# Optimization experiments

Measured on AMD Instinct MI355X. Metric: run time of the kernel, lower is better.

The kernel has to match this reference:

```python
import jax, jax.numpy as jnp
import numpy as np

T = 1 << 20  # hash-table size for bilateral-grid vertices
PRIMES = jnp.array([73856093, 19349663, 83492791, 49979687, 24036583], dtype=jnp.int32)
RGB2YUV = jnp.array([[0.299, 0.587, 0.114], [-0.168736, -0.331264, 0.5], [0.5, -0.418688, -0.081312]], dtype=jnp.float32)
YUV_OFF = jnp.array([0.0, 128.0, 128.0], dtype=jnp.float32)
SIG = jnp.array([8.0, 2.0, 2.0], dtype=jnp.float32)  # sigma_luma, sigma_chroma, sigma_chroma (mode=0)
SIGMA_SPATIAL = 7.0
LAM = 200.0
A_DIAG_MIN = 1e-5
CG_MAXITER = 12
BISTO_ITERS = 10
EPS = 1e-12
DIM = 5


def _hash(c):  # (..., 5) int32 -> flat bin id in [0, T)
    return (c * PRIMES).sum(-1) & (T - 1)


def _norm_max(x):
    s = jnp.clip(jnp.max(x, axis=(1, 2, 3), keepdims=True), 1e-5, 1.0)
    return x / s


def _conv(x, w, b, stride, pad):
    y = jax.lax.conv_general_dilated(x, w, (stride, stride), ((pad, pad), (pad, pad)), dimension_numbers=('NCHW', 'OIHW', 'NCHW'))
    return y + b[None, :, None, None]


def _gn(x, g, b, groups=2, eps=1e-5):
    B, C, H, W = x.shape
    xg = x.reshape(B, groups, -1)
    mu = xg.mean(-1, keepdims=True)
    var = xg.var(-1, keepdims=True)
    xg = (xg - mu) * jax.lax.rsqrt(var + eps)
    return xg.reshape(B, C, H, W) * g[None, :, None, None] + b[None, :, None, None]


def _reppad(x):
    return jnp.pad(x, ((0, 0), (0, 0), (1, 1), (1, 1)), mode='edge')


def _resize(x, h, w):
    B, C = x.shape[:2]
    return jax.image.resize(x, (B, C, h, w), method='linear')


def _bilateral_solve(guide_hwc, target_hwc, conf_hw):
    # fast bilateral solver (Barron & Poole): splat -> bistochastize -> PCG on grid -> slice
    H, W, C = target_hwc.shape
    N = H * W
    yuv = guide_hwc.reshape(N, 3) @ RGB2YUV.T + YUV_OFF
    yy, xx = jnp.meshgrid(jnp.arange(H, dtype=jnp.float32), jnp.arange(W, dtype=jnp.float32), indexing='ij')
    sp = jnp.stack([xx, yy], -1).reshape(N, 2) / SIGMA_SPATIAL
    coords = jnp.concatenate([jnp.floor(sp), jnp.floor(yuv / SIG)], -1).astype(jnp.int32)  # (N,5)
    h = _hash(coords)
    occ = jnp.zeros((T,), bool).at[h].set(True)
    ctab = jnp.full((T, 5), -1, jnp.int32).at[h].set(coords)
    # precompute 1-2-1 blur neighbor gathers along each of the 5 grid dims
    nhs, vals = [], []
    for d in range(DIM):
        for off in (-1, 1):
            nc = ctab.at[:, d].add(off)
            nh = _hash(nc)
            nhs.append(nh)
            vals.append(occ & occ[nh] & jnp.all(ctab[nh] == nc, axis=-1))
    occf = occ[:, None]

    def blur(v):  # (T,k)
        out = (2.0 * DIM) * v
        for nh, va in zip(nhs, vals):
            out = out + jnp.where(va[:, None], v[nh], 0.0)
        return jnp.where(occf, out, 0.0)

    def splat(v):  # (N,k) -> (T,k)
        return jax.ops.segment_sum(v, h, num_segments=T)

    # bistochastization
    m = splat(jnp.ones((N, 1), jnp.float32))
    n = occf.astype(jnp.float32)
    for _ in range(BISTO_ITERS):
        n = jnp.sqrt(n * m / (blur(n) + EPS))
    m = n * blur(n)

    w = conf_hw.reshape(N, 1)
    w_splat = splat(w)
    b = splat(w * target_hwc.reshape(N, C))
    y0 = b / (w_splat + EPS)
    A_diag = jnp.maximum(LAM * (m - (2.0 * DIM) * n * n) + w_splat, A_DIAG_MIN)
    Minv = 1.0 / A_diag

    def A(v):  # A = lam*(Dm - Dn B Dn) + diag(splat(w))
        return LAM * (m * v - n * blur(n * v)) + w_splat * v

    x0 = y0
    r0 = b - A(x0)
    z0 = Minv * r0

    def step(st, _):
        x, r, z, p = st
        Ap = A(p)
        rz = (r * z).sum(0)
        alpha = rz / ((p * Ap).sum(0) + EPS)
        x = x + alpha * p
        r = r - alpha * Ap
        z = Minv * r
        beta = (r * z).sum(0) / (rz + EPS)
        p = z + beta * p
        return (x, r, z, p), None

    (x, _, _, _), _ = jax.lax.scan(step, (x0, r0, z0, z0), None, length=CG_MAXITER)
    return x[h].reshape(H, W, C)  # slice


def _forward(image, feature, pred, w1, b1, g1, be1, w2, b2, g2, be2, wd1, bd1, gd1, bed1, wd2, bd2, gd2, bed2, wf, bf):
    image = _norm_max(image)
    feature = _norm_max(feature)
    inp = jax.lax.stop_gradient(jnp.concatenate([image, pred], axis=1))
    x1 = jax.nn.relu(_gn(_conv(_reppad(inp), w1, b1, 2, 0), g1, be1))
    x2 = jax.nn.relu(_gn(_conv(_reppad(x1), w2, b2, 2, 0), g2, be2))
    dx1 = jax.nn.relu(_gn(_conv(x2, wd1, bd1, 1, 1), gd1, bed1))
    dx1 = _resize(dx1, x1.shape[2], x1.shape[3])
    dx2 = jax.nn.relu(_gn(_conv(jnp.concatenate([dx1, x1], 1), wd2, bd2, 1, 1), gd2, bed2))
    dx2 = _resize(dx2, inp.shape[2], inp.shape[3])
    conf = 0.5 * (jnp.tanh(_conv(_reppad(dx2), wf, bf, 1, 0)) + 1.0)
    conf = conf / jnp.maximum(conf.max(), 1e-5)
    guide = jax.lax.stop_gradient(feature) * 255.0
    out = jax.vmap(_bilateral_solve)(guide.transpose(0, 2, 3, 1), pred.transpose(0, 2, 3, 1), conf[:, 0])
    return out.transpose(0, 3, 1, 2), conf


def setup_inputs():
    key = jax.random.key(0)
    ks = jax.random.split(key, 8)
    B, H, W = 2, 384, 512

    def cw(k, shape, fan_in):
        return jax.random.normal(k, shape, jnp.float32) * (1.0 / np.sqrt(fan_in))

    return {
        'image': jax.random.uniform(ks[0], (B, 3, H, W), jnp.float32),
        'feature': jax.random.uniform(ks[1], (B, 3, H, W), jnp.float32),
        'pred': jax.random.uniform(ks[2], (B, 3, H, W), jnp.float32),
        'w1': cw(ks[3], (16, 6, 4, 4), 6 * 16), 'b1': jnp.zeros((16,), jnp.float32),
        'g1': jnp.ones((16,), jnp.float32), 'be1': jnp.zeros((16,), jnp.float32),
        'w2': cw(ks[4], (16, 16, 4, 4), 16 * 16), 'b2': jnp.zeros((16,), jnp.float32),
        'g2': jnp.ones((16,), jnp.float32), 'be2': jnp.zeros((16,), jnp.float32),
        'wd1': cw(ks[5], (16, 16, 3, 3), 16 * 9), 'bd1': jnp.zeros((16,), jnp.float32),
        'gd1': jnp.ones((16,), jnp.float32), 'bed1': jnp.zeros((16,), jnp.float32),
        'wd2': cw(ks[6], (16, 32, 3, 3), 32 * 9), 'bd2': jnp.zeros((16,), jnp.float32),
        'gd2': jnp.ones((16,), jnp.float32), 'bed2': jnp.zeros((16,), jnp.float32),
        'wf': cw(ks[7], (1, 16, 3, 3), 16 * 9), 'bf': jnp.zeros((1,), jnp.float32),
    }


def reference(image, feature, pred, w1, b1, g1, be1, w2, b2, g2, be2, wd1, bd1, gd1, bed1, wd2, bd2, gd2, bed2, wf, bf):
    return _forward(image, feature, pred, w1, b1, g1, be1, w2, b2, g2, be2, wd1, bd1, gd1, bed1, wd2, bd2, gd2, bed2, wf, bf)
```

## Files before the change

### kernel.cpp

```cpp
#include <hip/hip_runtime.h>

#define H_ 384
#define W_ 512
#define N_ (H_*W_)
#define B_ 2
#define T_ 1048576
#define TMASK_ 0xFFFFFu
#define G2N_ ((2*N_)/256)
#define G2T_ ((2*T_)/256)
#define CHS_ 64
#define RZ0_ 192
#define RZB_ 2688
#define PAP0_ 5568
#define PAPB_ 2496
#define GN0_ 10560

__device__ __forceinline__ int prime(int d){
  switch(d){
    case 0: return 73856093;
    case 1: return 19349663;
    case 2: return 83492791;
    case 3: return 49979687;
    default: return 24036583;
  }
}

__device__ __forceinline__ float clampScale(float s){ return fminf(fmaxf(s,1e-5f),1.0f); }

__device__ __forceinline__ double blockReduceD(double v){
  __shared__ double sh[4];
  for(int s=32;s>0;s>>=1) v += __shfl_down(v,s,64);
  int lane=threadIdx.x&63, w=threadIdx.x>>6;
  if(lane==0) sh[w]=v;
  __syncthreads();
  double r = sh[0]+sh[1]+sh[2]+sh[3];
  __syncthreads();
  return r;
}
__device__ __forceinline__ float blockReduceMaxF(float v){
  __shared__ float sh[4];
  for(int s=32;s>0;s>>=1) v = fmaxf(v,__shfl_down(v,s,64));
  int lane=threadIdx.x&63, w=threadIdx.x>>6;
  if(lane==0) sh[w]=v;
  __syncthreads();
  float r = fmaxf(fmaxf(sh[0],sh[1]),fmaxf(sh[2],sh[3]));
  __syncthreads();
  return r;
}

__device__ __forceinline__ void redAdd(double* base, int c, double v){
  atomicAdd(&base[c*CHS_ + ((blockIdx.x&7)<<3)], v);
}
__device__ __forceinline__ float redSum(const double* base, int c){
  double s=0.0;
  #pragma unroll
  for(int j=0;j<8;j++) s += base[c*CHS_ + j*8];
  return (float)s;
}

__device__ __forceinline__ void gnStats(const double* acc, int b, int c, double len,
                                        float* mf, float* rs){
  const double* ba = acc + (b*2 + (c>>3))*128;
  double s=0.0,s2=0.0;
  #pragma unroll
  for(int j=0;j<8;j++){ s+=ba[j*8]; s2+=ba[64+j*8]; }
  double mean = s/len;
  double var = s2/len - mean*mean;
  *rs = (float)(1.0/sqrt(var + 1e-5));
  *mf = (float)mean;
}


__global__ __launch_bounds__(256) void k_maxes(const float4* img4, const float4* feat4, float* scal){
  const int PB = (3*N_)/4;
  for(int b=0;b<2;b++){
    float lm=0.f, lf=0.f;
    for(int idx = blockIdx.x*256+threadIdx.x; idx<PB; idx += gridDim.x*256){
      float4 a=img4[(size_t)b*PB+idx], c=feat4[(size_t)b*PB+idx];
      lm=fmaxf(lm, fmaxf(fmaxf(a.x,a.y),fmaxf(a.z,a.w)));
      lf=fmaxf(lf, fmaxf(fmaxf(c.x,c.y),fmaxf(c.z,c.w)));
    }
    lm=blockReduceMaxF(lm); lf=blockReduceMaxF(lf);
    if(threadIdx.x==0){
      atomicMax((int*)&scal[b],   __float_as_int(lm));
      atomicMax((int*)&scal[2+b], __float_as_int(lf));
    }
  }
}

template<int PLANE4>
__global__ __launch_bounds__(256) void k_gnrelu(const float4* in, float4* out, const double* acc,
                                                const float* gamma, const float* beta){
  int idx = blockIdx.x*256 + threadIdx.x;
  int t = idx / PLANE4;
  int c = t & 15, b = t >> 4;
  __shared__ float smf, srs, sg, sbe;
  if(threadIdx.x==0){
    float mf, rs;
    gnStats(acc, b, c, 8.0*(double)(PLANE4*4), &mf, &rs);
    smf=mf; srs=rs; sg=gamma[c]; sbe=beta[c];
  }
  __syncthreads();
  float mf=smf, rs=srs, g=sg, be=sbe;
  float4 v = in[idx];
  v.x = fmaxf((v.x-mf)*rs*g+be, 0.f);
  v.y = fmaxf((v.y-mf)*rs*g+be, 0.f);
  v.z = fmaxf((v.z-mf)*rs*g+be, 0.f);
  v.w = fmaxf((v.w-mf)*rs*g+be, 0.f);
  out[idx] = v;
}

template<bool SCALEA,int NCH,int K,int S,bool EDGE,int IH,int IW,int NOC>
__device__ __forceinline__ void conv_accum(const float* __restrict__ plane0, int icBase, float mulA,
                                           int oy, int ox, const float* wlds, float acc[NOC]){
  for(int ic=0; ic<NCH; ic++){
    const float* plane = plane0 + (size_t)ic*IH*IW;
    #pragma unroll
    for(int ky=0;ky<K;ky++){
      int iy = oy*S + ky - 1;
      int cy = min(max(iy,0),IH-1);
      bool yin = (iy>=0)&&(iy<IH);
      const float* row = plane + cy*IW;
      #pragma unroll
      for(int kx=0;kx<K;kx++){
        int ix = ox*S + kx - 1;
        float v;
        if(EDGE){
          int cx = min(max(ix,0),IW-1);
          v = row[cx];
          if(SCALEA) v = v * mulA;
        } else {
          bool inb = yin && ix>=0 && ix<IW;
          if(inb){
            v = row[ix];
            if(SCALEA) v = v * mulA;
          } else v = 0.f;
        }
        const float* wp = &wlds[((icBase+ic)*K*K + ky*K + kx)*NOC];
        #pragma unroll
        for(int q=0;q<NOC;q++) acc[q] += v*wp[q];
      }
    }
  }
}

template<bool SCALEA,int ICA,int ICB,int K,int S,bool EDGE,int IH,int IW,int OH,int OW,int OCSPLIT>
__global__ __launch_bounds__(256) void k_convT(const float* __restrict__ inA, const float* __restrict__ inB,
                        const float* __restrict__ wt, const float* __restrict__ bias,
                        float* __restrict__ out, double* gnaccOut, const float* scal){
  constexpr int IC = ICA+ICB;
  constexpr int NOC = 16/OCSPLIT;
  constexpr int PB = (B_*OH*OW)/256;
  __shared__ float wlds[IC*K*K*NOC];
  __shared__ float blds[NOC];
  int pb  = blockIdx.x % PB;
  int ocg = blockIdx.x / PB;
  int ocBase = ocg*NOC;
  for(int i=threadIdx.x; i<IC*K*K*NOC; i+=256){
    int q = i % NOC, ickk = i / NOC;
    wlds[i] = wt[(ocBase+q)*IC*K*K + ickk];
  }
  if(threadIdx.x<NOC) blds[threadIdx.x]=bias[ocBase+threadIdx.x];
  __syncthreads();
  int idx = pb*256+threadIdx.x;
  int ox = idx % OW; int t=idx/OW; int oy=t%OH; int b=t/OH;
  float mulA = SCALEA ? 1.0f/clampScale(scal[b]) : 1.0f;
  float acc[NOC];
  #pragma unroll
  for(int q=0;q<NOC;q++) acc[q]=0.f;
  conv_accum<SCALEA,ICA,K,S,EDGE,IH,IW,NOC>(inA + (size_t)b*ICA*IH*IW, 0, mulA, oy, ox, wlds, acc);
  if constexpr(ICB>0)
    conv_accum<false,(ICB>0?ICB:1),K,S,EDGE,IH,IW,NOC>(inB + (size_t)b*ICB*IH*IW, ICA, 1.0f, oy, ox, wlds, acc);
  double s=0.0,s2=0.0;
  #pragma unroll
  for(int q=0;q<NOC;q++){
    float vv = acc[q] + blds[q];
    out[(((size_t)b*16+(ocBase+q))*OH+oy)*OW+ox] = vv;
    s += vv; s2 += (double)vv*(double)vv;
  }
  s=blockReduceD(s); s2=blockReduceD(s2);
  if(threadIdx.x==0){
    int grp = ocBase>>3;
    int sub = (blockIdx.x&7)<<3;
    atomicAdd(&gnaccOut[(b*2+grp)*128 + sub],      s);
    atomicAdd(&gnaccOut[(b*2+grp)*128 + 64 + sub], s2);
  }
}

template<int IH,int IW>
__global__ __launch_bounds__(256) void k_resize2x(const float* __restrict__ in, float* __restrict__ out,
                                                  const double* acc, const float* gamma, const float* beta){
  constexpr int QP = IH*IW;
  constexpr int OW = 2*IW;
  int idx = blockIdx.x*256 + threadIdx.x;
  int q = idx % QP; int t = idx / QP;
  int qx = q % IW, qy = q / IW;
  int c = t & 15, b = t >> 4;
  __shared__ float smf, srs, sg, sbe;
  if(threadIdx.x==0){
    float mf, rs;
    gnStats(acc, b, c, 8.0*(double)QP, &mf, &rs);
    smf=mf; srs=rs; sg=gamma[c]; sbe=beta[c];
  }
  __syncthreads();
  float mf=smf, rs=srs, g=sg, be=sbe;
  const float* plane = in + (size_t)t*QP;
  int ym = max(qy-1,0), yp = min(qy+1,IH-1);
  int xm = max(qx-1,0), xp = min(qx+1,IW-1);
  const float* r0 = plane + ym*IW;
  const float* r1 = plane + qy*IW;
  const float* r2 = plane + yp*IW;
  float a00=fmaxf((r0[xm]-mf)*rs*g+be,0.f), a01=fmaxf((r0[qx]-mf)*rs*g+be,0.f), a02=fmaxf((r0[xp]-mf)*rs*g+be,0.f);
  float a10=fmaxf((r1[xm]-mf)*rs*g+be,0.f), a11=fmaxf((r1[qx]-mf)*rs*g+be,0.f), a12=fmaxf((r1[xp]-mf)*rs*g+be,0.f);
  float a20=fmaxf((r2[xm]-mf)*rs*g+be,0.f), a21=fmaxf((r2[qx]-mf)*rs*g+be,0.f), a22=fmaxf((r2[xp]-mf)*rs*g+be,0.f);
  float e0 = 0.25f*a00+0.75f*a01, o0 = 0.75f*a01+0.25f*a02;
  float e1 = 0.25f*a10+0.75f*a11, o1 = 0.75f*a11+0.25f*a12;
  float e2 = 0.25f*a20+0.75f*a21, o2 = 0.75f*a21+0.25f*a22;
  float2 rE = make_float2(0.25f*e0+0.75f*e1, 0.25f*o0+0.75f*o1);
  float2 rO = make_float2(0.75f*e1+0.25f*e2, 0.75f*o1+0.25f*o2);
  float* po = out + (size_t)t*(4*QP) + (size_t)(2*qy)*OW + 2*qx;
  *(float2*)po        = rE;
  *(float2*)(po + OW) = rO;
}

__global__ __launch_bounds__(256) void k_conv5(const float* in, const float* wf, const float* bf,
                                               float* confr, float* scal){
  int idx = blockIdx.x*256 + threadIdx.x;
  int ph = idx % (N_/2); int b = idx / (N_/2);
  int oyh = ph / W_, ox = ph % W_;
  int oy0 = oyh*2;
  float acc0 = bf[0], acc1 = bf[0];
  for(int ic=0; ic<16; ic++){
    const float* plane = in + ((size_t)b*16+ic)*N_;
    #pragma unroll
    for(int ky=0;ky<3;ky++){
      int iy0 = min(max(oy0+ky-1,0),H_-1);
      int iy1 = min(max(oy0+ky,0),H_-1);
      const float* row0 = plane + iy0*W_;
      const float* row1 = plane + iy1*W_;
      #pragma unroll
      for(int kx=0;kx<3;kx++){
        int ix = min(max(ox+kx-1,0),W_-1);
        float w = wf[(ic*3+ky)*3+kx];
        acc0 += row0[ix]*w;
        acc1 += row1[ix]*w;
      }
    }
  }
  float c0 = 0.5f*(tanhf(acc0)+1.0f);
  float c1 = 0.5f*(tanhf(acc1)+1.0f);
  confr[(size_t)b*N_ + oy0*W_ + ox]     = c0;
  confr[(size_t)b*N_ + (oy0+1)*W_ + ox] = c1;
  float mx = blockReduceMaxF(fmaxf(c0,c1));
  if(threadIdx.x==0) atomicMax((int*)&scal[4], __float_as_int(mx));
}


__global__ __launch_bounds__(256) void k_px1(const float* feat, const float* scal,
                                             int* hpix, int2* cpix2, int* winner,
                                             float* mcompE, float4* splatE4){
  int idx = blockIdx.x*256 + threadIdx.x;
  int b = idx / N_, pix = idx % N_;
  int y = pix / W_, x = pix % W_;
  mcompE[idx] = 0.f;
  splatE4[idx] = make_float4(0.f,0.f,0.f,0.f);
  float sF = clampScale(scal[2+b]);
  const float* fb = feat + (size_t)b*3*N_;
  float R  = __fmul_rn(__fdiv_rn(fb[pix],      sF), 255.0f);
  float G  = __fmul_rn(__fdiv_rn(fb[N_+pix],   sF), 255.0f);
  float Bl = __fmul_rn(__fdiv_rn(fb[2*N_+pix], sF), 255.0f);
  float Y = __fadd_rn(__fadd_rn(__fadd_rn(__fmul_rn(0.299f,R),     __fmul_rn(0.587f,G)),  __fmul_rn(0.114f,Bl)), 0.0f);
  float U = __fadd_rn(__fadd_rn(__fadd_rn(__fmul_rn(-0.168736f,R), __fmul_rn(-0.331264f,G)), __fmul_rn(0.5f,Bl)), 128.0f);
  float V = __fadd_rn(__fadd_rn(__fadd_rn(__fmul_rn(0.5f,R),       __fmul_rn(-0.418688f,G)), __fmul_rn(-0.081312f,Bl)), 128.0f);
  int c[5];
  c[0] = (int)floorf(__fdiv_rn((float)x, 7.0f));
  c[1] = (int)floorf(__fdiv_rn((float)y, 7.0f));
  c[2] = (int)floorf(__fdiv_rn(Y, 8.0f));
  c[3] = (int)floorf(__fdiv_rn(U, 2.0f));
  c[4] = (int)floorf(__fdiv_rn(V, 2.0f));
  unsigned hh = 0;
  #pragma unroll
  for(int d=0;d<5;d++) hh += (unsigned)c[d]*(unsigned)prime(d);
  hh &= TMASK_;
  hpix[idx]=(int)hh;
  cpix2[idx]=make_int2(c[0] | (c[1]<<10) | (c[2]<<20), c[3] | (c[4]<<10));
  atomicMax(&winner[(size_t)b*T_+(int)hh], pix);
}


__global__ __launch_bounds__(256) void k_cnt(const int* winner, int* bcnt){
  int t = blockIdx.x*256 + threadIdx.x;
  bool occ = winner[t] >= 0;
  __shared__ int wc[4];
  unsigned long long mk = __ballot(occ);
  int lane = threadIdx.x & 63, w = threadIdx.x >> 6;
  if(lane==0) wc[w] = __popcll(mk);
  __syncthreads();
  if(threadIdx.x==0) bcnt[blockIdx.x] = wc[0]+wc[1]+wc[2]+wc[3];
}

__global__ __launch_bounds__(256) void k_scan(const int* bcnt, int* boff, int* count){
  __shared__ int ssum[256];
  int t = threadIdx.x;
  int base = t*32;
  int loc[32];
  int s=0;
  #pragma unroll
  for(int j=0;j<32;j++){ loc[j]=s; s+=bcnt[base+j]; }
  int mys = s;
  ssum[t]=s;
  __syncthreads();
  for(int st=1; st<128; st<<=1){
    int add = ((t&127) >= st) ? ssum[t-st] : 0;
    __syncthreads();
    ssum[t] += add;
    __syncthreads();
  }
  int excl = ssum[t] - mys;
  #pragma unroll
  for(int j=0;j<32;j++) boff[base+j] = excl + loc[j];
  if(t==127) count[0]=ssum[127];
  if(t==255) count[1]=ssum[255];
}

__global__ __launch_bounds__(256) void k_cmp(const int* winner, const int* boff,
                                             int2* cidx2, int* slot_of){
  int t = blockIdx.x*256 + threadIdx.x;
  int b = t / T_;
  int wn = winner[t];
  bool occ = wn >= 0;
  __shared__ int wc[4];
  unsigned long long mk = __ballot(occ);
  int lane = threadIdx.x & 63, w = threadIdx.x >> 6;
  if(lane==0) wc[w] = __popcll(mk);
  __syncthreads();
  int wpre = 0;
  for(int k2=0;k2<4;k2++) if(k2<w) wpre += wc[k2];
  if(occ){
    int li = boff[blockIdx.x] + wpre + __popcll(mk & ((1ull<<lane)-1ull));
    int gi = b*N_ + li;
    cidx2[t] = make_int2(gi, wn);
    slot_of[gi] = t - b*T_;
  } else {
    cidx2[t] = make_int2(-1, -1);
  }
}

__global__ __launch_bounds__(256) void k_px3(int* hpix_gpix, const int2* cidx2, const float* confr,
                                             const float* scal, float* confout, const float* pred,
                                             float* mcomp, float4* splat4, float* mcompE, float* splatE){
  int idx = blockIdx.x*256 + threadIdx.x;
  int b = idx / N_, pix = idx % N_;
  int2 cw = cidx2[(size_t)b*T_ + hpix_gpix[idx]];
  int gi = cw.x;
  hpix_gpix[idx] = gi;
  float w = confr[idx] / fmaxf(scal[4], 1e-5f);
  confout[idx] = w;
  const float* pb = pred + (size_t)b*3*N_;
  float v0 = __fmul_rn(w, pb[pix]);
  float v1 = __fmul_rn(w, pb[N_+pix]);
  float v2 = __fmul_rn(w, pb[2*N_+pix]);
  if(cw.y == pix){
    splat4[gi] = make_float4(v0,v1,v2,w);
    mcomp[gi] = 1.0f;
  } else {
    float* s = splatE + 4*(size_t)gi;
    atomicAdd(s+0, v0);
    atomicAdd(s+1, v1);
    atomicAdd(s+2, v2);
    atomicAdd(s+3, w);
    atomicAdd(&mcompE[gi], 1.0f);
  }
}


__global__ __launch_bounds__(256) void k_bisto0(const int* count, const int* slot_of,
                      const int2* cpix2, const int2* cidx2, int* nbr,
                      float* mcomp, const float* mcompE, float4* splat4, const float4* splatE4,
                      float* nd){
  int i = blockIdx.x*256 + threadIdx.x;
  int b = i / N_, li = i - b*N_;
  if(li >= count[b]) return;
  int hh = slot_of[i];
  const int2* c2b = cidx2 + (size_t)b*T_;
  int2 cself = c2b[hh];
  int2 cp = cpix2[(size_t)b*N_ + cself.y];
  float4 sp = splat4[i]; float4 se = splatE4[i];
  sp.x+=se.x; sp.y+=se.y; sp.z+=se.z; sp.w+=se.w;
  splat4[i]=sp;
  float mTot = mcomp[i] + mcompE[i];
  mcomp[i]=mTot;
  float bv = 10.f;
  #pragma unroll
  for(int j=0;j<10;j++){
    int d=j>>1; int off=(j&1)?1:-1;
    unsigned nh = ((unsigned)hh + (unsigned)(off*prime(d))) & TMASK_;
    int nb = -1;
    int2 cn2 = c2b[nh];
    if(cn2.y>=0){
      int2 cn = cpix2[(size_t)b*N_ + cn2.y];
      int e0 = cp.x + (d==0?off: d==1?off*(1<<10) : d==2?off*(1<<20) : 0);
      int e1 = cp.y + (d==3?off: d==4?off*(1<<10) : 0);
      if(cn.x==e0 && cn.y==e1) nb = cn2.x;
    }
    nbr[(size_t)j*(2*N_)+i]=nb;
    if(nb>=0) bv += 1.0f;
  }
  nd[i] = sqrtf(1.0f*mTot/(bv+1e-12f));
}

__global__ __launch_bounds__(256) void k_bisto(const int* count, const int* nbr,
                                               const float* ns, float* nd, const float* mc){
  int i = blockIdx.x*256 + threadIdx.x;
  int b = i / N_, li = i - b*N_;
  if(li >= count[b]) return;
  float nv = ns[i];
  float bv = 10.f*nv;
  #pragma unroll
  for(int j=0;j<10;j++){
    int nb = nbr[(size_t)j*(2*N_)+i];
    if(nb>=0) bv += ns[nb];
  }
  nd[i] = sqrtf(nv*mc[i]/(bv+1e-12f));
}

__global__ __launch_bounds__(256) void k_Ar0(const int* count, const int* nbr, const float* n,
                      const float4* splat4, float4* meta4, float4* x4, float4* rS, float4* zp0,
                      double* rz0){
  int i = blockIdx.x*256 + threadIdx.x;
  int b = i / N_, li = i - b*N_;
  double a0=0.0,a1=0.0,a2=0.0;
  if(li < count[b]){
    float4 vb4 = splat4[i];
    float wsi = vb4.w;
    float nv = n[i];
    float x0 = vb4.x/(wsi+1e-12f);
    float x1 = vb4.y/(wsi+1e-12f);
    float x2 = vb4.z/(wsi+1e-12f);
    float bv = 10.f*nv;
    float s0=10.f*(nv*x0), s1=10.f*(nv*x1), s2=10.f*(nv*x2);
    #pragma unroll
    for(int j=0;j<10;j++){
      int nb = nbr[(size_t)j*(2*N_)+i];
      if(nb>=0){
        float4 vbn = splat4[nb];
        float nn = n[nb];
        bv += nn;
        s0 += nn*(vbn.x/(vbn.w+1e-12f));
        s1 += nn*(vbn.y/(vbn.w+1e-12f));
        s2 += nn*(vbn.z/(vbn.w+1e-12f));
      }
    }
    float mfin = nv*bv;
    float Ad = fmaxf(200.0f*(mfin - 10.f*nv*nv) + wsi, 1e-5f);
    float mi = 1.0f/Ad;
    float A0 = 200.f*(mfin*x0 - nv*s0) + wsi*x0;
    float A1 = 200.f*(mfin*x1 - nv*s1) + wsi*x1;
    float A2 = 200.f*(mfin*x2 - nv*s2) + wsi*x2;
    float r0v = vb4.x-A0, r1v = vb4.y-A1, r2v = vb4.z-A2;
    float z0=mi*r0v, z1=mi*r1v, z2=mi*r2v;
    meta4[i]=make_float4(nv,mfin,wsi,mi);
    x4[i]=make_float4(x0,x1,x2,0.f);
    rS[i]=make_float4(r0v,r1v,r2v,mi);
    zp0[2*(size_t)i]   = make_float4(z0,z1,z2,mi);
    zp0[2*(size_t)i+1] = make_float4(z0,z1,z2,nv);
    a0=(double)r0v*z0; a1=(double)r1v*z1; a2=(double)r2v*z2;
  }
  a0=blockReduceD(a0); a1=blockReduceD(a1); a2=blockReduceD(a2);
  if(threadIdx.x==0){
    double* base = rz0 + b*RZB_;
    redAdd(base,0,a0); redAdd(base,1,a1); redAdd(base,2,a2);
  }
}

__global__ __launch_bounds__(256) void k_Ap(const int* count, const int* nbr, const float4* meta4,
                     const float4* __restrict__ zpCur, float4* __restrict__ zpNext, float4* Ap4,
                     const double* bNum, const double* bDen, int bstr, double* pAp){
  int i = blockIdx.x*256 + threadIdx.x;
  int b = (blockIdx.x*256) / N_;
  int li = i - b*N_;
  __shared__ float sbe[3];
  if(threadIdx.x==0){
    if(bstr==0){ sbe[0]=0.f; sbe[1]=0.f; sbe[2]=0.f; }
    else{
      const double* nB_ = bNum + b*bstr;
      const double* dB_ = bDen + b*bstr;
      #pragma unroll
      for(int c=0;c<3;c++) sbe[c] = redSum(nB_,c) / (redSum(dB_,c)+1e-12f);
    }
  }
  __syncthreads();
  float be0=sbe[0], be1=sbe[1], be2=sbe[2];
  double a0=0.0,a1=0.0,a2=0.0;
  if(li < count[b]){
    float4 mt = meta4[i];
    float nv = mt.x, mfin = mt.y, wsi = mt.z;
    float4 zs = zpCur[2*(size_t)i];
    float4 ps = zpCur[2*(size_t)i+1];
    float p0 = zs.x + be0*ps.x;
    float p1 = zs.y + be1*ps.y;
    float p2 = zs.z + be2*ps.z;
    float s0=10.f*(nv*p0), s1=10.f*(nv*p1), s2=10.f*(nv*p2);
    #pragma unroll
    for(int j=0;j<10;j++){
      int nb = nbr[(size_t)j*(2*N_)+i];
      if(nb>=0){
        float4 zn = zpCur[2*(size_t)nb];
        float4 pn = zpCur[2*(size_t)nb+1];
        float nn = pn.w;
        s0 += nn*(zn.x + be0*pn.x);
        s1 += nn*(zn.y + be1*pn.y);
        s2 += nn*(zn.z + be2*pn.z);
      }
    }
    float A0 = 200.f*(mfin*p0 - nv*s0) + wsi*p0;
    float A1 = 200.f*(mfin*p1 - nv*s1) + wsi*p1;
    float A2 = 200.f*(mfin*p2 - nv*s2) + wsi*p2;
    zpNext[2*(size_t)i+1]=make_float4(p0,p1,p2,nv);
    Ap4[i]=make_float4(A0,A1,A2,0.f);
    a0=(double)p0*A0; a1=(double)p1*A1; a2=(double)p2*A2;
  }
  a0=blockReduceD(a0); a1=blockReduceD(a1); a2=blockReduceD(a2);
  if(threadIdx.x==0){
    double* base = pAp + b*PAPB_;
    redAdd(base,0,a0); redAdd(base,1,a1); redAdd(base,2,a2);
  }
}

__global__ __launch_bounds__(256) void k_upd1(const int* count, float4* x4, float4* rS,
                       const float4* __restrict__ zpNext_p, float4* __restrict__ zpNext_z,
                       const float4* Ap4,
                       const double* rzCur, const double* pApC, double* rzNew, int doRz){
  int i = blockIdx.x*256 + threadIdx.x;
  int b = (blockIdx.x*256) / N_;
  int li = i - b*N_;
  __shared__ float sal[3];
  if(threadIdx.x==0){
    const double* rc = rzCur + b*RZB_;
    const double* pc = pApC  + b*PAPB_;
    #pragma unroll
    for(int c=0;c<3;c++) sal[c] = redSum(rc,c) / (redSum(pc,c)+1e-12f);
  }
  __syncthreads();
  float al0=sal[0], al1=sal[1], al2=sal[2];
  double a0=0.0,a1=0.0,a2=0.0;
  if(li < count[b]){
    float4 xv = x4[i];
    float4 rv = rS[i];
    float4 pv = zpNext_p[2*(size_t)i+1];
    float4 av = Ap4[i];
    float mi = rv.w;
    float x0=xv.x+al0*pv.x, x1=xv.y+al1*pv.y, x2=xv.z+al2*pv.z;
    float r0v=rv.x-al0*av.x, r1v=rv.y-al1*av.y, r2v=rv.z-al2*av.z;
    float z0=mi*r0v, z1=mi*r1v, z2=mi*r2v;
    x4[i]=make_float4(x0,x1,x2,0.f);
    rS[i]=make_float4(r0v,r1v,r2v,mi);
    zpNext_z[2*(size_t)i]=make_float4(z0,z1,z2,mi);
    a0=(double)r0v*z0; a1=(double)r1v*z1; a2=(double)r2v*z2;
  }
  if(doRz){
    a0=blockReduceD(a0); a1=blockReduceD(a1); a2=blockReduceD(a2);
    if(threadIdx.x==0){
      double* base = rzNew + b*RZB_;
      redAdd(base,0,a0); redAdd(base,1,a1); redAdd(base,2,a2);
    }
  }
}

__global__ __launch_bounds__(256) void k_out(const float4* x4, const int* gpix, float* out){
  int idx = blockIdx.x*256 + threadIdx.x;
  int b = idx / N_, pix = idx % N_;
  float4 xv = x4[gpix[idx]];
  out[((size_t)(b*3+0))*N_+pix] = xv.x;
  out[((size_t)(b*3+1))*N_+pix] = xv.y;
  out[((size_t)(b*3+2))*N_+pix] = xv.z;
}


extern "C" void kernel_launch(void* const* d_in, const int* in_sizes, int n_in,
                              void* d_out, int out_size, void* d_ws, size_t ws_size,
                              hipStream_t stream){
  const float* image=(const float*)d_in[0];
  const float* feature=(const float*)d_in[1];
  const float* pred=(const float*)d_in[2];
  const float* w1=(const float*)d_in[3];  const float* b1=(const float*)d_in[4];
  const float* g1=(const float*)d_in[5];  const float* be1=(const float*)d_in[6];
  const float* w2=(const float*)d_in[7];  const float* b2=(const float*)d_in[8];
  const float* g2=(const float*)d_in[9];  const float* be2=(const float*)d_in[10];
  const float* wd1=(const float*)d_in[11];const float* bd1=(const float*)d_in[12];
  const float* gd1=(const float*)d_in[13];const float* bed1=(const float*)d_in[14];
  const float* wd2=(const float*)d_in[15];const float* bd2=(const float*)d_in[16];
  const float* gd2=(const float*)d_in[17];const float* bed2=(const float*)d_in[18];
  const float* wf=(const float*)d_in[19]; const float* bf=(const float*)d_in[20];
  float* outp=(float*)d_out;
  float* confout = outp + (size_t)B_*3*N_;

  char* wsb=(char*)d_ws;
  float* scal=(float*)wsb;
  int* count=(int*)(wsb+256);
  double* scalD=(double*)(wsb+4096);
  double* zeroD = scalD;
  auto rzArr  = [&](int it)->double*{ return scalD + RZ0_  + it*192; };
  auto pApArr = [&](int it)->double*{ return scalD + PAP0_ + it*192; };
  auto gnAcc  = [&](int L)->double*{ return scalD + GN0_ + L*512; };

  size_t off = 131072;
  auto alloc=[&](size_t bytes)->char*{ char* pp=wsb+off; off=(off+bytes+255)&~(size_t)255; return pp; };
  const size_t ALLOC0 = off;

  float* x1   =(float*)alloc((size_t)B_*16*192*256*4);
  float* x1n  =(float*)alloc((size_t)B_*16*192*256*4);
  float* x2   =(float*)alloc((size_t)B_*16*96*128*4);
  float* x2n  =(float*)alloc((size_t)B_*16*96*128*4);
  float* dx1  =(float*)alloc((size_t)B_*16*96*128*4);
  float* dx1r =(float*)alloc((size_t)B_*16*192*256*4);
  float* dx2  =(float*)alloc((size_t)B_*16*192*256*4);
  float* dx2r =(float*)alloc((size_t)B_*16*N_*4);

  off = ALLOC0;
  int*    winner =(int*)   alloc((size_t)2*T_*4);
  int2*   cidx2  =(int2*)  alloc((size_t)2*T_*8);
  int*    hpix   =(int*)   alloc((size_t)2*N_*4);
  int2*   cpix2  =(int2*)  alloc((size_t)2*N_*8);
  int*    slot_of=(int*)   alloc((size_t)2*N_*4);
  int*    nbr    =(int*)   alloc((size_t)2*N_*10*4);
  float*  mcomp  =(float*) alloc((size_t)2*N_*4);
  float4* splat4 =(float4*)alloc((size_t)2*N_*16);
  float*  mcompE =(float*) alloc((size_t)2*N_*4);
  float*  splatE =(float*) alloc((size_t)2*N_*16);
  float*  nA     =(float*) alloc((size_t)2*N_*4);
  float*  nB     =(float*) alloc((size_t)2*N_*4);
  float4* meta4  =(float4*)alloc((size_t)2*N_*16);
  float4* x4     =(float4*)alloc((size_t)2*N_*16);
  float4* rS     =(float4*)alloc((size_t)2*N_*16);
  float4* zpA4   =(float4*)alloc((size_t)2*N_*32);
  float4* zpB4   =(float4*)alloc((size_t)2*N_*32);
  int*    bcnt   =(int*)   alloc((size_t)G2T_*4);
  int*    boff   =(int*)   alloc((size_t)G2T_*4);
  float4* Ap4    = splat4;
  float*  confr  = (float*)zpB4;

  dim3 blk(256);

  hipMemsetAsync(wsb, 0, 4096 + 12608*8, stream);

  k_maxes<<<128,blk,0,stream>>>((const float4*)image,(const float4*)feature,scal);

  k_convT<true,3,3,4,2,true,384,512,192,256,4><<<4*((B_*192*256)/256),blk,0,stream>>>(
      image,pred,w1,b1,x1,gnAcc(0),scal);
  k_gnrelu<12288><<<(B_*16*12288)/256,blk,0,stream>>>((const float4*)x1,(float4*)x1n,gnAcc(0),g1,be1);
  k_convT<false,16,0,4,2,true,192,256,96,128,8><<<8*((B_*96*128)/256),blk,0,stream>>>(
      x1n,x1n,w2,b2,x2,gnAcc(1),scal);
  k_gnrelu<3072><<<(B_*16*3072)/256,blk,0,stream>>>((const float4*)x2,(float4*)x2n,gnAcc(1),g2,be2);
  k_convT<false,16,0,3,1,false,96,128,96,128,8><<<8*((B_*96*128)/256),blk,0,stream>>>(
      x2n,x2n,wd1,bd1,dx1,gnAcc(2),scal);
  k_resize2x<96,128><<<(B_*16*96*128)/256,blk,0,stream>>>(dx1, dx1r, gnAcc(2), gd1, bed1);
  k_convT<false,16,16,3,1,false,192,256,192,256,4><<<4*((B_*192*256)/256),blk,0,stream>>>(
      dx1r,x1n,wd2,bd2,dx2,gnAcc(3),scal);
  k_resize2x<192,256><<<(B_*16*192*256)/256,blk,0,stream>>>(dx2, dx2r, gnAcc(3), gd2, bed2);

  k_conv5<<<(B_*(N_/2))/256,blk,0,stream>>>(dx2r, wf, bf, confr, scal);

  hipMemsetAsync(winner, 0xFF, (size_t)2*T_*4, stream);
  k_px1<<<G2N_,blk,0,stream>>>(feature,scal,hpix,cpix2,winner,mcompE,(float4*)splatE);
  k_cnt<<<G2T_,blk,0,stream>>>(winner,bcnt);
  k_scan<<<1,blk,0,stream>>>(bcnt,boff,count);
  k_cmp<<<G2T_,blk,0,stream>>>(winner,boff,cidx2,slot_of);
  k_px3<<<G2N_,blk,0,stream>>>(hpix,cidx2,confr,scal,confout,pred,mcomp,splat4,mcompE,splatE);

  k_bisto0<<<G2N_,blk,0,stream>>>(count,slot_of,cpix2,cidx2,nbr,mcomp,mcompE,splat4,(const float4*)splatE,nA);
  for(int it=1; it<10; ++it){
    float* src = (it&1) ? nA : nB;
    float* dst = (it&1) ? nB : nA;
    k_bisto<<<G2N_,blk,0,stream>>>(count,nbr,src,dst,mcomp);
  }
  float* nfin = nB;

  k_Ar0<<<G2N_,blk,0,stream>>>(count,nbr,nfin,splat4,meta4,x4,rS,zpA4,rzArr(0));

  float4* zp[2]={zpA4,zpB4};
  for(int it=0; it<12; ++it){
    float4* zpCur  = zp[it&1];
    float4* zpNext = zp[(it+1)&1];
    const double* bN = (it==0) ? zeroD : rzArr(it);
    const double* bD = (it==0) ? zeroD : rzArr(it-1);
    int bstr = (it==0) ? 0 : RZB_;
    k_Ap<<<G2N_,blk,0,stream>>>(count,nbr,meta4,zpCur,zpNext,Ap4,bN,bD,bstr,pApArr(it));
    k_upd1<<<G2N_,blk,0,stream>>>(count,x4,rS,zpNext,zpNext,Ap4,rzArr(it),pApArr(it),rzArr(it+1),(it<11)?1:0);
  }
  k_out<<<G2N_,blk,0,stream>>>(x4,hpix,outp);

  (void)in_sizes; (void)n_in; (void)out_size; (void)ws_size;
}
```

Baseline: 699.1 us.

## Fuse final CG update into output gather and winner init into conv5

The last PCG iteration's x update is folded into the output kernel: it computes alpha from the final rz/pAp sums and adds alpha*p only at the gathered slots, so the final k_upd1 launch is skipped. The memset of the winner table is moved into k_conv5 via int4 stores, removing a separate fill pass. Two mid-size convolutions also get a larger split factor (8 to 16 blocks per tile) to raise parallelism. This relies on zpA4 holding the final p after 12 iterations and on conv5's grid covering the whole winner table.

```diff
diff --git a/kernel.cpp b/kernel.cpp
--- a/kernel.cpp
+++ b/kernel.cpp
@@ -224,8 +224,13 @@
 }
 
 __global__ __launch_bounds__(256) void k_conv5(const float* in, const float* wf, const float* bf,
-                                               float* confr, float* scal){
+                                               float* confr, float* scal, int4* winner4){
   int idx = blockIdx.x*256 + threadIdx.x;
+  #pragma unroll
+  for(int j=0;j<3;j++){
+    int w4 = idx + j*((B_*(N_/2))/1);
+    if(w4 < (2*T_)/4) winner4[w4] = make_int4(-1,-1,-1,-1);
+  }
   int ph = idx % (N_/2); int b = idx / (N_/2);
   int oyh = ph / W_, ox = ph % W_;
   int oy0 = oyh*2;
@@ -530,7 +535,7 @@
 __global__ __launch_bounds__(256) void k_upd1(const int* count, float4* x4, float4* rS,
                        const float4* __restrict__ zpNext_p, float4* __restrict__ zpNext_z,
                        const float4* Ap4,
-                       const double* rzCur, const double* pApC, double* rzNew, int doRz){
+                       const double* rzCur, const double* pApC, double* rzNew){
   int i = blockIdx.x*256 + threadIdx.x;
   int b = (blockIdx.x*256) / N_;
   int li = i - b*N_;
@@ -558,22 +563,32 @@
     zpNext_z[2*(size_t)i]=make_float4(z0,z1,z2,mi);
     a0=(double)r0v*z0; a1=(double)r1v*z1; a2=(double)r2v*z2;
   }
-  if(doRz){
-    a0=blockReduceD(a0); a1=blockReduceD(a1); a2=blockReduceD(a2);
-    if(threadIdx.x==0){
-      double* base = rzNew + b*RZB_;
-      redAdd(base,0,a0); redAdd(base,1,a1); redAdd(base,2,a2);
-    }
-  }
-}
-
-__global__ __launch_bounds__(256) void k_out(const float4* x4, const int* gpix, float* out){
+  a0=blockReduceD(a0); a1=blockReduceD(a1); a2=blockReduceD(a2);
+  if(threadIdx.x==0){
+    double* base = rzNew + b*RZB_;
+    redAdd(base,0,a0); redAdd(base,1,a1); redAdd(base,2,a2);
+  }
+}
+
+__global__ __launch_bounds__(256) void k_out(const float4* x4, const float4* __restrict__ zpFin,
+                                             const int* gpix, float* out,
+                                             const double* rzCur, const double* pApC){
   int idx = blockIdx.x*256 + threadIdx.x;
   int b = idx / N_, pix = idx % N_;
-  float4 xv = x4[gpix[idx]];
-  out[((size_t)(b*3+0))*N_+pix] = xv.x;
-  out[((size_t)(b*3+1))*N_+pix] = xv.y;
-  out[((size_t)(b*3+2))*N_+pix] = xv.z;
+  __shared__ float sal[3];
+  if(threadIdx.x==0){
+    const double* rc = rzCur + b*RZB_;
+    const double* pc = pApC  + b*PAPB_;
+    #pragma unroll
+    for(int c=0;c<3;c++) sal[c] = redSum(rc,c) / (redSum(pc,c)+1e-12f);
+  }
+  __syncthreads();
+  int gi = gpix[idx];
+  float4 xv = x4[gi];
+  float4 pv = zpFin[2*(size_t)gi+1];
+  out[((size_t)(b*3+0))*N_+pix] = xv.x + sal[0]*pv.x;
+  out[((size_t)(b*3+1))*N_+pix] = xv.y + sal[1]*pv.y;
+  out[((size_t)(b*3+2))*N_+pix] = xv.z + sal[2]*pv.z;
 }
 
 
@@ -649,19 +664,18 @@
   k_convT<true,3,3,4,2,true,384,512,192,256,4><<<4*((B_*192*256)/256),blk,0,stream>>>(
       image,pred,w1,b1,x1,gnAcc(0),scal);
   k_gnrelu<12288><<<(B_*16*12288)/256,blk,0,stream>>>((const float4*)x1,(float4*)x1n,gnAcc(0),g1,be1);
-  k_convT<false,16,0,4,2,true,192,256,96,128,8><<<8*((B_*96*128)/256),blk,0,stream>>>(
+  k_convT<false,16,0,4,2,true,192,256,96,128,16><<<16*((B_*96*128)/256),blk,0,stream>>>(
       x1n,x1n,w2,b2,x2,gnAcc(1),scal);
   k_gnrelu<3072><<<(B_*16*3072)/256,blk,0,stream>>>((const float4*)x2,(float4*)x2n,gnAcc(1),g2,be2);
-  k_convT<false,16,0,3,1,false,96,128,96,128,8><<<8*((B_*96*128)/256),blk,0,stream>>>(
+  k_convT<false,16,0,3,1,false,96,128,96,128,16><<<16*((B_*96*128)/256),blk,0,stream>>>(
       x2n,x2n,wd1,bd1,dx1,gnAcc(2),scal);
   k_resize2x<96,128><<<(B_*16*96*128)/256,blk,0,stream>>>(dx1, dx1r, gnAcc(2), gd1, bed1);
   k_convT<false,16,16,3,1,false,192,256,192,256,4><<<4*((B_*192*256)/256),blk,0,stream>>>(
       dx1r,x1n,wd2,bd2,dx2,gnAcc(3),scal);
   k_resize2x<192,256><<<(B_*16*192*256)/256,blk,0,stream>>>(dx2, dx2r, gnAcc(3), gd2, bed2);
 
-  k_conv5<<<(B_*(N_/2))/256,blk,0,stream>>>(dx2r, wf, bf, confr, scal);
-
-  hipMemsetAsync(winner, 0xFF, (size_t)2*T_*4, stream);
+  k_conv5<<<(B_*(N_/2))/256,blk,0,stream>>>(dx2r, wf, bf, confr, scal, (int4*)winner);
+
   k_px1<<<G2N_,blk,0,stream>>>(feature,scal,hpix,cpix2,winner,mcompE,(float4*)splatE);
   k_cnt<<<G2T_,blk,0,stream>>>(winner,bcnt);
   k_scan<<<1,blk,0,stream>>>(bcnt,boff,count);
@@ -686,9 +700,10 @@
     const double* bD = (it==0) ? zeroD : rzArr(it-1);
     int bstr = (it==0) ? 0 : RZB_;
     k_Ap<<<G2N_,blk,0,stream>>>(count,nbr,meta4,zpCur,zpNext,Ap4,bN,bD,bstr,pApArr(it));
-    k_upd1<<<G2N_,blk,0,stream>>>(count,x4,rS,zpNext,zpNext,Ap4,rzArr(it),pApArr(it),rzArr(it+1),(it<11)?1:0);
-  }
-  k_out<<<G2N_,blk,0,stream>>>(x4,hpix,outp);
+    if(it<11)
+      k_upd1<<<G2N_,blk,0,stream>>>(count,x4,rS,zpNext,zpNext,Ap4,rzArr(it),pApArr(it),rzArr(it+1));
+  }
+  k_out<<<G2N_,blk,0,stream>>>(x4,zpA4,hpix,outp,rzArr(11),pApArr(11));
 
   (void)in_sizes; (void)n_in; (void)out_size; (void)ws_size;
 }
```

Result: no change. 710.8 us (+1.7%).
